# Kernel optimization log

Measured on AMD Instinct MI355X. Metric: run time of the kernel, lower is better.

Reference implementation:

```python
import jax, jax.numpy as jnp
import numpy as np

N_NODES = 50000
N_EDGES = 1600000
NUM_GRAPHS = 512
NEG_SLOPE = 0.2


def _glorot(key, shape):
    fan_in, fan_out = shape[0], shape[-1]
    lim = jnp.sqrt(6.0 / (fan_in + fan_out))
    return jax.random.uniform(key, shape, jnp.float32, -lim, lim)


def setup_inputs() -> dict:
    key = jax.random.key(0)
    ks = jax.random.split(key, 10)
    x = jax.random.normal(ks[0], (N_NODES, 133), jnp.float32)
    edge_index = jax.random.randint(ks[1], (2, N_EDGES), 0, N_NODES, jnp.int64)
    batch = jnp.sort(jax.random.randint(ks[2], (N_NODES,), 0, NUM_GRAPHS, jnp.int64))
    # conv1: GATConv(133 -> 8, heads=8, concat=True)
    W1 = _glorot(ks[3], (133, 64))
    att_src1 = _glorot(ks[4], (8, 8))   # [H, C]
    att_dst1 = _glorot(ks[5], (8, 8))
    b1 = jnp.zeros((64,), jnp.float32)
    # conv2: GATConv(64 -> 2, heads=1, concat=True)
    W2 = _glorot(ks[6], (64, 2))
    att_src2 = _glorot(ks[7], (1, 2))
    att_dst2 = _glorot(ks[8], (1, 2))
    b2 = jnp.zeros((2,), jnp.float32)
    return {"x": x, "edge_index": edge_index, "batch": batch,
            "W1": W1, "att_src1": att_src1, "att_dst1": att_dst1, "b1": b1,
            "W2": W2, "att_src2": att_src2, "att_dst2": att_dst2, "b2": b2}


def gat_conv(x, src, dst, W, att_src, att_dst, bias):
    """PyG GATConv (add_self_loops already applied via src/dst), concat=True, eval mode."""
    N = x.shape[0]
    H, C = att_src.shape
    h = (x @ W).reshape(N, H, C)                      # [N, H, C]
    a_src = jnp.sum(h * att_src[None], axis=-1)       # [N, H]
    a_dst = jnp.sum(h * att_dst[None], axis=-1)       # [N, H]
    e = a_src[src] + a_dst[dst]                       # [E, H]
    e = jnp.where(e > 0, e, NEG_SLOPE * e)            # leaky_relu
    # segment softmax over incoming edges of each dst node
    e_max = jax.ops.segment_max(e, dst, num_segments=N)  # [N, H]
    e_exp = jnp.exp(e - e_max[dst])
    denom = jax.ops.segment_sum(e_exp, dst, num_segments=N)
    alpha = e_exp / jnp.maximum(denom, 1e-16)[dst]    # [E, H]
    msg = h[src] * alpha[:, :, None]                  # [E, H, C]
    out = jax.ops.segment_sum(msg, dst, num_segments=N)  # [N, H, C]
    return out.reshape(N, H * C) + bias


def reference(x, edge_index, batch, W1, att_src1, att_dst1, b1, W2, att_src2, att_dst2, b2):
    N = x.shape[0]
    loops = jnp.arange(N, dtype=edge_index.dtype)
    src = jnp.concatenate([edge_index[0], loops])
    dst = jnp.concatenate([edge_index[1], loops])
    # dropout layers are identity in eval mode
    h = gat_conv(x, src, dst, W1, att_src1, att_dst1, b1)   # [N, 64]
    h = jax.nn.elu(h)
    h = gat_conv(h, src, dst, W2, att_src2, att_dst2, b2)   # [N, 2]
    out = jax.ops.segment_sum(h, batch, num_segments=NUM_GRAPHS)  # [G, 2]
    return out
```

## Files before the change

### kernel.cpp

```cpp
#include <hip/hip_runtime.h>
#include <hip/hip_fp16.h>

#define NN 50000
#define NE 1600000
#define NG 512
#define NEG 0.2f

#define NBKT 782
#define CHUNK 8192
#define NSB ((NE + CHUNK - 1) / CHUNK)
#define CAP 3072
#define NBL 782
#define NSLOT 32

typedef _Float16 half8 __attribute__((ext_vector_type(8)));
typedef float f32x4 __attribute__((ext_vector_type(4)));


__global__ __launch_bounds__(256) void k_init(const float* __restrict__ W1,
                                              _Float16* __restrict__ W1f,
                                              int* __restrict__ bcursor,
                                              float* __restrict__ out) {
    int i = blockIdx.x * 256 + threadIdx.x;
    if (i < 1280) {
        int f = i >> 6, l = i & 63;
        int kt = f >> 2, ct = f & 3;
        int g = l >> 4, c16 = l & 15;
#pragma unroll
        for (int j = 0; j < 8; ++j) {
            int k = kt * 32 + g * 8 + j;
            float v = (k < 133) ? W1[k * 64 + ct * 16 + c16] : 0.f;
            W1f[i * 8 + j] = (_Float16)v;
        }
    } else if (i < 1280 + NBKT * 16) {
        bcursor[i - 1280] = 0;
    } else if (i < 1280 + NBKT * 16 + NG * 2) {
        out[i - 1280 - NBKT * 16] = 0.f;
    }
}

__global__ __launch_bounds__(256) void k_mfma_scatter(const float* __restrict__ x,
                                                      const _Float16* __restrict__ W1f,
                                                      const float* __restrict__ attS,
                                                      const float* __restrict__ attD,
                                                      __half* __restrict__ h1h,
                                                      float* __restrict__ aS,
                                                      float* __restrict__ aD,
                                                      const int* __restrict__ ei,
                                                      int* __restrict__ bcursor,
                                                      unsigned* __restrict__ binned) {
    if (blockIdx.x < NBL) {
        const int wid = (blockIdx.x * 256 + threadIdx.x) >> 6;
        const int nb  = wid * 16;
        if (nb >= NN) return;
        const int l   = threadIdx.x & 63;
        const int g   = l >> 4, c16 = l & 15;
        const long xbase = (long)(nb + c16) * 133;

        half8 bfr[5][4];
#pragma unroll
        for (int kt = 0; kt < 5; ++kt)
#pragma unroll
            for (int ct = 0; ct < 4; ++ct)
                bfr[kt][ct] = *reinterpret_cast<const half8*>(W1f + ((kt * 4 + ct) * 64 + l) * 8);

        f32x4 acc[4] = {{0.f,0.f,0.f,0.f},{0.f,0.f,0.f,0.f},{0.f,0.f,0.f,0.f},{0.f,0.f,0.f,0.f}};
#pragma unroll
        for (int kt = 0; kt < 5; ++kt) {
            half8 a;
#pragma unroll
            for (int i = 0; i < 8; ++i) {
                int k = kt * 32 + g * 8 + i;
                a[i] = (_Float16)((k < 133) ? x[xbase + k] : 0.f);
            }
#pragma unroll
            for (int ct = 0; ct < 4; ++ct)
                acc[ct] = __builtin_amdgcn_mfma_f32_16x16x32_f16(a, bfr[kt][ct], acc[ct], 0, 0, 0);
        }

#pragma unroll
        for (int ct = 0; ct < 4; ++ct) {
            const int col  = ct * 16 + c16;
            const int head = col >> 3;
            const float as_w = attS[head * 8 + (col & 7)];
            const float ad_w = attD[head * 8 + (col & 7)];
#pragma unroll
            for (int r = 0; r < 4; ++r) {
                const int n = nb + g * 4 + r;
                float v = acc[ct][r];
                h1h[n * 64 + col] = __float2half(v);
                float ps = v * as_w, pd = v * ad_w;
                ps += __shfl_xor(ps, 1, 64); pd += __shfl_xor(pd, 1, 64);
                ps += __shfl_xor(ps, 2, 64); pd += __shfl_xor(pd, 2, 64);
                ps += __shfl_xor(ps, 4, 64); pd += __shfl_xor(pd, 4, 64);
                if ((l & 7) == 0) {
                    aS[n * 8 + head] = ps;
                    aD[n * 8 + head] = pd;
                }
            }
        }
    } else {
        __shared__ int hist[NBKT];
        __shared__ int basel[NBKT];
        const int t = threadIdx.x;
        const int estart = (blockIdx.x - NBL) * CHUNK;

        for (int i = t; i < NBKT; i += 256) hist[i] = 0;
        __syncthreads();

        unsigned pk[32];
        int br[32];
#pragma unroll
        for (int i = 0; i < 32; ++i) {
            int e = estart + t + i * 256;
            if (e < NE) {
                int s = ei[e];
                int d = ei[NE + e];
                int b = d >> 6;
                int r = atomicAdd(&hist[b], 1);
                pk[i] = ((unsigned)s << 6) | (unsigned)(d & 63);
                br[i] = (r << 10) | b;
            } else {
                br[i] = -1;
            }
        }
        __syncthreads();
        for (int i = t; i < NBKT; i += 256)
            basel[i] = hist[i] ? (i * CAP + atomicAdd(&bcursor[i * 16], hist[i])) : 0;
        __syncthreads();
#pragma unroll
        for (int i = 0; i < 32; ++i) {
            if (br[i] >= 0) {
                int b = br[i] & 1023;
                int r = br[i] >> 10;
                int pos = basel[b] + r;
                if (pos < (b + 1) * CAP) binned[pos] = pk[i];
            }
        }
    }
}

__global__ __launch_bounds__(256) void k_buildcsr(const unsigned* __restrict__ binned,
                                                  const int* __restrict__ bcursor,
                                                  int2* __restrict__ row_se,
                                                  unsigned short* __restrict__ csr) {
    __shared__ unsigned edg[CAP];
    __shared__ unsigned short csrl[CAP];
    __shared__ int deg[64], scn[64], cur[64];

    const int b = blockIdx.x, t = threadIdx.x;
    const int ebase = b * CAP;
    const int ecnt  = min(bcursor[b * 16], CAP);
    const int nbase = b << 6;
    const int ncnt  = min(64, NN - nbase);

    for (int i = t; i < ecnt; i += 256) edg[i] = binned[ebase + i];
    if (t < 64) deg[t] = 0;
    __syncthreads();
    for (int i = t; i < ecnt; i += 256) atomicAdd(&deg[edg[i] & 63], 1);
    __syncthreads();
    if (t < 64) scn[t] = deg[t];
    __syncthreads();
    for (int o = 1; o < 64; o <<= 1) {
        int v = (t < 64 && t >= o) ? scn[t - o] : 0;
        __syncthreads();
        if (t < 64) scn[t] += v;
        __syncthreads();
    }
    if (t < 64) {
        cur[t] = scn[t] - deg[t];
        if (t < ncnt) row_se[nbase + t] = make_int2(ebase + scn[t] - deg[t], ebase + scn[t]);
    }
    __syncthreads();
    for (int i = t; i < ecnt; i += 256) {
        unsigned pk = edg[i];
        int pos = atomicAdd(&cur[pk & 63], 1);
        csrl[pos] = (unsigned short)(pk >> 6);
    }
    __syncthreads();
    for (int i = t; i < ecnt; i += 256) csr[ebase + i] = csrl[i];
}

__global__ __launch_bounds__(256) void k_gather1(const unsigned short* __restrict__ csr,
                                                 const int2* __restrict__ row_se,
                                                 const float* __restrict__ aS,
                                                 const float* __restrict__ aD,
                                                 const unsigned* __restrict__ h1u,
                                                 const float* __restrict__ b1,
                                                 const float* __restrict__ W2,
                                                 const float* __restrict__ attS2,
                                                 const float* __restrict__ attD2,
                                                 float4* __restrict__ node4) {
    __shared__ float exs[4][64 * 8];
    __shared__ int   svs[4][64];

    const int sub  = threadIdx.x >> 6;
    const int lane = threadIdx.x & 63;
    const int n    = (blockIdx.x * 256 + threadIdx.x) >> 6;
    const int hp   = lane & 7;
    const int ebl  = lane >> 3;
    const int half = lane >> 5;
    const int c    = lane & 31;
    const int hc   = c >> 2;

    const float aDhp = aD[n * 8 + hp];
    const int2 se = row_se[n];
    const int e0 = se.x, e1 = se.y;

    float2 acc = make_float2(0.f, 0.f);
    float den = 0.f;
    for (int base = e0; base < e1; base += 64) {
        const int cnt = min(64, e1 - base);
        int sv = (base + lane < e1) ? (int)csr[base + lane] : n;
        svs[sub][lane] = sv;

#pragma unroll
        for (int p = 0; p < 8; ++p) {
            int eb = p * 8 + ebl;
            int s  = svs[sub][eb];
            float ev = aS[s * 8 + hp] + aDhp;
            ev = fmaxf(ev, NEG * ev);
            float ex = __expf(ev);
            if (eb >= cnt) ex = 0.f;
            exs[sub][eb * 8 + hp] = ex;
            den += ex;
        }

        const int cnt8 = (cnt + 7) & ~7;
        for (int eb = 0; eb < cnt8; eb += 8) {
#pragma unroll
            for (int k = 0; k < 8; k += 2) {
                int   e2 = eb + k + half;
                int   s  = svs[sub][e2];
                float ex = exs[sub][e2 * 8 + hc];
                unsigned hv = h1u[s * 32 + c];
                float2 f2 = __half22float2(*reinterpret_cast<__half2*>(&hv));
                acc.x = fmaf(ex, f2.x, acc.x);
                acc.y = fmaf(ex, f2.y, acc.y);
            }
        }
    }
    den += __shfl_xor(den, 8, 64);
    den += __shfl_xor(den, 16, 64);
    den += __shfl_xor(den, 32, 64);
    float ev_s = aS[n * 8 + hp] + aDhp;
    ev_s = fmaxf(ev_s, NEG * ev_s);
    float ex_self = __expf(ev_s);
    den += ex_self;

    acc.x += __shfl_xor(acc.x, 32, 64);
    acc.y += __shfl_xor(acc.y, 32, 64);

    float den_c = __shfl(den, hc, 64);
    float ex_sc = __shfl(ex_self, hc, 64);

    unsigned hvs = h1u[n * 32 + c];
    float2 fs = __half22float2(*reinterpret_cast<__half2*>(&hvs));
    float inv = 1.f / fmaxf(den_c, 1e-16f);
    float2 bb = reinterpret_cast<const float2*>(b1)[c];
    float vx = fmaf(ex_sc, fs.x, acc.x) * inv + bb.x;
    float vy = fmaf(ex_sc, fs.y, acc.y) * inv + bb.y;
    vx = vx > 0.f ? vx : (__expf(vx) - 1.f);
    vy = vy > 0.f ? vy : (__expf(vy) - 1.f);

    float4 w = reinterpret_cast<const float4*>(W2)[c];
    float p0 = vx * w.x + vy * w.z;
    float p1 = vx * w.y + vy * w.w;
    p0 += __shfl_xor(p0, 1, 64);  p1 += __shfl_xor(p1, 1, 64);
    p0 += __shfl_xor(p0, 2, 64);  p1 += __shfl_xor(p1, 2, 64);
    p0 += __shfl_xor(p0, 4, 64);  p1 += __shfl_xor(p1, 4, 64);
    p0 += __shfl_xor(p0, 8, 64);  p1 += __shfl_xor(p1, 8, 64);
    p0 += __shfl_xor(p0, 16, 64); p1 += __shfl_xor(p1, 16, 64);
    if (lane == 0) {
        float s2 = p0 * attS2[0] + p1 * attS2[1];
        float d2 = p0 * attD2[0] + p1 * attD2[1];
        node4[n] = make_float4(p0, p1, s2, d2);
    }
}

__global__ __launch_bounds__(256) void k_gather2(const unsigned short* __restrict__ csr,
                                                 const int2* __restrict__ row_se,
                                                 const float4* __restrict__ node4,
                                                 const int* __restrict__ batch,
                                                 const float* __restrict__ b2,
                                                 float* __restrict__ out) {
    __shared__ float pool[NSLOT][2];
    __shared__ int gbase_s;
    const int t = threadIdx.x;
    const int n = blockIdx.x * 256 + t;

    if (t == 0) gbase_s = batch[blockIdx.x * 256];
    for (int i = t; i < NSLOT * 2; i += 256) (&pool[0][0])[i] = 0.f;
    __syncthreads();

    if (n < NN) {
        const float4 vn = node4[n];
        const float aDd = vn.w;

        float ev = vn.z + aDd;
        ev = fmaxf(ev, NEG * ev);
        float ex = __expf(ev);
        float den = ex, p0 = ex * vn.x, p1 = ex * vn.y;

        const int2 se = row_se[n];
#pragma unroll 4
        for (int e = se.x; e < se.y; ++e) {
            int s = csr[e];
            float4 vs = node4[s];
            float ev2 = vs.z + aDd;
            ev2 = fmaxf(ev2, NEG * ev2);
            float ex2 = __expf(ev2);
            den += ex2;
            p0 = fmaf(ex2, vs.x, p0);
            p1 = fmaf(ex2, vs.y, p1);
        }
        float inv = 1.f / fmaxf(den, 1e-16f);
        float v0 = p0 * inv + b2[0];
        float v1 = p1 * inv + b2[1];

        int g = batch[n];
        int slot = g - gbase_s;
        if (slot < NSLOT) {
            atomicAdd(&pool[slot][0], v0);
            atomicAdd(&pool[slot][1], v1);
        } else {
            atomicAdd(&out[g * 2 + 0], v0);
            atomicAdd(&out[g * 2 + 1], v1);
        }
    }
    __syncthreads();
    for (int i = t; i < NSLOT; i += 256) {
        float v0 = pool[i][0], v1 = pool[i][1];
        if (v0 != 0.f || v1 != 0.f) {
            int g = gbase_s + i;
            atomicAdd(&out[g * 2 + 0], v0);
            atomicAdd(&out[g * 2 + 1], v1);
        }
    }
}

extern "C" void kernel_launch(void* const* d_in, const int* in_sizes, int n_in,
                              void* d_out, int out_size, void* d_ws, size_t ws_size,
                              hipStream_t stream) {
    const float* x     = (const float*)d_in[0];
    const int*   ei    = (const int*)d_in[1];
    const int*   batch = (const int*)d_in[2];
    const float* W1    = (const float*)d_in[3];
    const float* attS1 = (const float*)d_in[4];
    const float* attD1 = (const float*)d_in[5];
    const float* b1    = (const float*)d_in[6];
    const float* W2    = (const float*)d_in[7];
    const float* attS2 = (const float*)d_in[8];
    const float* attD2 = (const float*)d_in[9];
    const float* b2    = (const float*)d_in[10];
    float* out = (float*)d_out;

    int* ws = (int*)d_ws;
    __half* h1h = (__half*)ws;
    unsigned* h1u = (unsigned*)ws;
    float* aS1 = (float*)(ws + (size_t)NN * 32);
    float* aD1 = (float*)(ws + (size_t)NN * 40);
    float4* node4 = (float4*)(ws + (size_t)NN * 48);
    int2* row_se  = (int2*)(ws + (size_t)NN * 52);
    int* bcursor  = ws + (size_t)NN * 54;
    _Float16* W1f = (_Float16*)(ws + (size_t)NN * 54 + 12544);
    unsigned* binned    = (unsigned*)(ws + (size_t)NN * 55);
    unsigned short* csr = (unsigned short*)(ws + (size_t)NN * 55 + (size_t)NBKT * CAP);

    k_init<<<(1280 + NBKT * 16 + NG * 2 + 255) / 256, 256, 0, stream>>>(W1, W1f, bcursor, out);
    k_mfma_scatter<<<NBL + NSB, 256, 0, stream>>>(x, W1f, attS1, attD1, h1h, aS1, aD1,
                                                  ei, bcursor, binned);
    k_buildcsr<<<NBKT, 256, 0, stream>>>(binned, bcursor, row_se, csr);
    k_gather1<<<NN / 4, 256, 0, stream>>>(csr, row_se, aS1, aD1, h1u, b1, W2,
                                          attS2, attD2, node4);
    k_gather2<<<(NN + 255) / 256, 256, 0, stream>>>(csr, row_se, node4, batch, b2, out);
}
```

Measured before the change: 100.0 us.

## Split fused MFMA/scatter kernel and use two-pass edge binning with smaller chunks

The fused kernel that ran the layer-1 MFMA projection in some blocks and edge binning in others becomes two separate kernel launches. The binning kernel now makes two passes over its chunk: first a histogram, then a re-read of the edges to scatter them. This replaces the 32-entry per-thread register arrays and cuts register pressure. The chunk size is halved, doubling the number of binning blocks. The trade-offs are an extra launch with serialization between the two kernels, re-reading edge indices, and more global cursor atomics.

```diff
diff --git a/kernel.cpp b/kernel.cpp
--- a/kernel.cpp
+++ b/kernel.cpp
@@ -7,10 +7,9 @@
 #define NEG 0.2f
 
 #define NBKT 782
-#define CHUNK 8192
+#define CHUNK 4096
 #define NSB ((NE + CHUNK - 1) / CHUNK)
 #define CAP 3072
-#define NBL 782
 #define NSLOT 32
 
 typedef _Float16 half8 __attribute__((ext_vector_type(8)));
@@ -39,104 +38,92 @@
     }
 }
 
-__global__ __launch_bounds__(256) void k_mfma_scatter(const float* __restrict__ x,
-                                                      const _Float16* __restrict__ W1f,
-                                                      const float* __restrict__ attS,
-                                                      const float* __restrict__ attD,
-                                                      __half* __restrict__ h1h,
-                                                      float* __restrict__ aS,
-                                                      float* __restrict__ aD,
-                                                      const int* __restrict__ ei,
-                                                      int* __restrict__ bcursor,
-                                                      unsigned* __restrict__ binned) {
-    if (blockIdx.x < NBL) {
-        const int wid = (blockIdx.x * 256 + threadIdx.x) >> 6;
-        const int nb  = wid * 16;
-        if (nb >= NN) return;
-        const int l   = threadIdx.x & 63;
-        const int g   = l >> 4, c16 = l & 15;
-        const long xbase = (long)(nb + c16) * 133;
-
-        half8 bfr[5][4];
-#pragma unroll
-        for (int kt = 0; kt < 5; ++kt)
-#pragma unroll
-            for (int ct = 0; ct < 4; ++ct)
-                bfr[kt][ct] = *reinterpret_cast<const half8*>(W1f + ((kt * 4 + ct) * 64 + l) * 8);
-
-        f32x4 acc[4] = {{0.f,0.f,0.f,0.f},{0.f,0.f,0.f,0.f},{0.f,0.f,0.f,0.f},{0.f,0.f,0.f,0.f}};
-#pragma unroll
-        for (int kt = 0; kt < 5; ++kt) {
-            half8 a;
-#pragma unroll
-            for (int i = 0; i < 8; ++i) {
-                int k = kt * 32 + g * 8 + i;
-                a[i] = (_Float16)((k < 133) ? x[xbase + k] : 0.f);
+__global__ __launch_bounds__(256) void k_linmfma(const float* __restrict__ x,
+                                                 const _Float16* __restrict__ W1f,
+                                                 const float* __restrict__ attS,
+                                                 const float* __restrict__ attD,
+                                                 __half* __restrict__ h1h,
+                                                 float* __restrict__ aS,
+                                                 float* __restrict__ aD) {
+    const int wid = (blockIdx.x * 256 + threadIdx.x) >> 6;
+    const int nb  = wid * 16;
+    if (nb >= NN) return;
+    const int l   = threadIdx.x & 63;
+    const int g   = l >> 4, c16 = l & 15;
+    const long xbase = (long)(nb + c16) * 133;
+
+    half8 bfr[5][4];
+#pragma unroll
+    for (int kt = 0; kt < 5; ++kt)
+#pragma unroll
+        for (int ct = 0; ct < 4; ++ct)
+            bfr[kt][ct] = *reinterpret_cast<const half8*>(W1f + ((kt * 4 + ct) * 64 + l) * 8);
+
+    f32x4 acc[4] = {{0.f,0.f,0.f,0.f},{0.f,0.f,0.f,0.f},{0.f,0.f,0.f,0.f},{0.f,0.f,0.f,0.f}};
+#pragma unroll
+    for (int kt = 0; kt < 5; ++kt) {
+        half8 a;
+#pragma unroll
+        for (int i = 0; i < 8; ++i) {
+            int k = kt * 32 + g * 8 + i;
+            a[i] = (_Float16)((k < 133) ? x[xbase + k] : 0.f);
+        }
+#pragma unroll
+        for (int ct = 0; ct < 4; ++ct)
+            acc[ct] = __builtin_amdgcn_mfma_f32_16x16x32_f16(a, bfr[kt][ct], acc[ct], 0, 0, 0);
+    }
+
+#pragma unroll
+    for (int ct = 0; ct < 4; ++ct) {
+        const int col  = ct * 16 + c16;
+        const int head = col >> 3;
+        const float as_w = attS[head * 8 + (col & 7)];
+        const float ad_w = attD[head * 8 + (col & 7)];
+#pragma unroll
+        for (int r = 0; r < 4; ++r) {
+            const int n = nb + g * 4 + r;
+            float v = acc[ct][r];
+            h1h[n * 64 + col] = __float2half(v);
+            float ps = v * as_w, pd = v * ad_w;
+            ps += __shfl_xor(ps, 1, 64); pd += __shfl_xor(pd, 1, 64);
+            ps += __shfl_xor(ps, 2, 64); pd += __shfl_xor(pd, 2, 64);
+            ps += __shfl_xor(ps, 4, 64); pd += __shfl_xor(pd, 4, 64);
+            if ((l & 7) == 0) {
+                aS[n * 8 + head] = ps;
+                aD[n * 8 + head] = pd;
             }
-#pragma unroll
-            for (int ct = 0; ct < 4; ++ct)
-                acc[ct] = __builtin_amdgcn_mfma_f32_16x16x32_f16(a, bfr[kt][ct], acc[ct], 0, 0, 0);
-        }
-
-#pragma unroll
-        for (int ct = 0; ct < 4; ++ct) {
-            const int col  = ct * 16 + c16;
-            const int head = col >> 3;
-            const float as_w = attS[head * 8 + (col & 7)];
-            const float ad_w = attD[head * 8 + (col & 7)];
-#pragma unroll
-            for (int r = 0; r < 4; ++r) {
-                const int n = nb + g * 4 + r;
-                float v = acc[ct][r];
-                h1h[n * 64 + col] = __float2half(v);
-                float ps = v * as_w, pd = v * ad_w;
-                ps += __shfl_xor(ps, 1, 64); pd += __shfl_xor(pd, 1, 64);
-                ps += __shfl_xor(ps, 2, 64); pd += __shfl_xor(pd, 2, 64);
-                ps += __shfl_xor(ps, 4, 64); pd += __shfl_xor(pd, 4, 64);
-                if ((l & 7) == 0) {
-                    aS[n * 8 + head] = ps;
-                    aD[n * 8 + head] = pd;
-                }
-            }
-        }
-    } else {
-        __shared__ int hist[NBKT];
-        __shared__ int basel[NBKT];
-        const int t = threadIdx.x;
-        const int estart = (blockIdx.x - NBL) * CHUNK;
-
-        for (int i = t; i < NBKT; i += 256) hist[i] = 0;
-        __syncthreads();
-
-        unsigned pk[32];
-        int br[32];
-#pragma unroll
-        for (int i = 0; i < 32; ++i) {
-            int e = estart + t + i * 256;
-            if (e < NE) {
-                int s = ei[e];
-                int d = ei[NE + e];
-                int b = d >> 6;
-                int r = atomicAdd(&hist[b], 1);
-                pk[i] = ((unsigned)s << 6) | (unsigned)(d & 63);
-                br[i] = (r << 10) | b;
-            } else {
-                br[i] = -1;
-            }
-        }
-        __syncthreads();
-        for (int i = t; i < NBKT; i += 256)
-            basel[i] = hist[i] ? (i * CAP + atomicAdd(&bcursor[i * 16], hist[i])) : 0;
-        __syncthreads();
-#pragma unroll
-        for (int i = 0; i < 32; ++i) {
-            if (br[i] >= 0) {
-                int b = br[i] & 1023;
-                int r = br[i] >> 10;
-                int pos = basel[b] + r;
-                if (pos < (b + 1) * CAP) binned[pos] = pk[i];
-            }
-        }
+        }
+    }
+}
+
+__global__ __launch_bounds__(256) void k_binscatter(const int* __restrict__ ei,
+                                                    int* __restrict__ bcursor,
+                                                    unsigned* __restrict__ binned) {
+    __shared__ int hist[NBKT];
+    __shared__ int basel[NBKT];
+    const int t = threadIdx.x;
+    const int estart = blockIdx.x * CHUNK;
+    const int eend = min(estart + CHUNK, NE);
+
+    for (int i = t; i < NBKT; i += 256) hist[i] = 0;
+    __syncthreads();
+    for (int e = estart + t; e < eend; e += 256)
+        atomicAdd(&hist[ei[NE + e] >> 6], 1);
+    __syncthreads();
+    for (int i = t; i < NBKT; i += 256) {
+        int h = hist[i];
+        basel[i] = h ? (i * CAP + atomicAdd(&bcursor[i * 16], h)) : 0;
+    }
+    __syncthreads();
+    for (int i = t; i < NBKT; i += 256) hist[i] = 0;
+    __syncthreads();
+    for (int e = estart + t; e < eend; e += 256) {
+        int s = ei[e];
+        int d = ei[NE + e];
+        int b = d >> 6;
+        int r = atomicAdd(&hist[b], 1);
+        int pos = basel[b] + r;
+        if (pos < (b + 1) * CAP) binned[pos] = ((unsigned)s << 6) | (unsigned)(d & 63);
     }
 }
 
@@ -368,8 +355,8 @@
     unsigned short* csr = (unsigned short*)(ws + (size_t)NN * 55 + (size_t)NBKT * CAP);
 
     k_init<<<(1280 + NBKT * 16 + NG * 2 + 255) / 256, 256, 0, stream>>>(W1, W1f, bcursor, out);
-    k_mfma_scatter<<<NBL + NSB, 256, 0, stream>>>(x, W1f, attS1, attD1, h1h, aS1, aD1,
-                                                  ei, bcursor, binned);
+    k_linmfma<<<(NN / 16 + 3) / 4, 256, 0, stream>>>(x, W1f, attS1, attD1, h1h, aS1, aD1);
+    k_binscatter<<<NSB, 256, 0, stream>>>(ei, bcursor, binned);
     k_buildcsr<<<NBKT, 256, 0, stream>>>(binned, bcursor, row_se, csr);
     k_gather1<<<NN / 4, 256, 0, stream>>>(csr, row_se, aS1, aD1, h1u, b1, W2,
                                           attS2, attD2, node4);
```

Result: slower. 118.9 us (+18.8%).
